# Optimization experiments

Hardware: AMD Instinct MI355X
Metric: run time of the kernel (lower is better)

## Reference

```python
import jax, jax.numpy as jnp
import numpy as np

RADIUS = 0.2
NSAMPLE = 32
BANDWIDTH = 0.1


def ellipsoid_query(xyz, new_xyz, radius, nsample):
    """xyz:(B,N,3), new_xyz:(B,P,3) -> idx:(B,P,nsample) int32.
    Ellipsoid semi-axes (radius, 2*radius, radius); first nsample hits,
    padded with the first hit (index 0 if empty), matching the CUDA kernel.
    """
    B, N, _ = xyz.shape
    inv_sq = jnp.asarray([1.0 / radius**2, 1.0 / (2.0 * radius) ** 2, 1.0 / radius**2],
                         dtype=xyz.dtype)
    # accumulate per-coordinate to avoid a (B,P,N,3) intermediate
    q = jnp.zeros((B, new_xyz.shape[1], N), dtype=xyz.dtype)
    for k in range(3):
        d = new_xyz[:, :, None, k] - xyz[:, None, :, k]  # (B,P,N)
        q = q + d * d * inv_sq[k]
    mask = q < 1.0
    cand = jnp.where(mask, jnp.arange(N, dtype=jnp.int32), jnp.int32(N))  # invalid -> N
    cand = jnp.sort(cand, axis=-1)[..., :nsample]                          # (B,P,S)
    first = cand[..., :1]
    first = jnp.where(first >= N, jnp.int32(0), first)
    return jnp.where(cand >= N, first, cand)


def group(features, idx):
    """features:(B,C,N), idx:(B,P,S) -> (B,C,P,S)"""
    return jnp.take_along_axis(features[:, :, None, :], idx[:, None, :, :], axis=-1)


def setup_inputs() -> dict:
    key = jax.random.key(0)
    k1, k2, k3 = jax.random.split(key, 3)
    xyz = jax.random.uniform(k1, (4, 8192, 3), dtype=jnp.float32)
    new_xyz = jax.random.uniform(k2, (4, 2048, 3), dtype=jnp.float32)
    features = jax.random.normal(k3, (4, 64, 8192), dtype=jnp.float32)
    return {"xyz": xyz, "new_xyz": new_xyz, "features": features}


def reference(xyz, new_xyz, features):
    idx = ellipsoid_query(xyz, new_xyz, RADIUS, NSAMPLE)          # (B,P,S)
    xyz_trans = jnp.transpose(xyz, (0, 2, 1))                      # (B,3,N)
    grouped_xyz = group(xyz_trans, idx)                            # (B,3,P,S)
    # density: gaussian of distance to center
    g = jnp.transpose(grouped_xyz, (0, 2, 3, 1))                   # (B,P,S,3)
    dist = jnp.linalg.norm(g - new_xyz[:, :, None, :], axis=-1)    # (B,P,S)
    density = jnp.exp(-dist**2 / (2.0 * BANDWIDTH**2)) / (2.5 * BANDWIDTH)
    grouped_density = (1.0 / density)[:, None, :, :]               # (B,1,P,S)
    grouped_features = group(features, idx)                        # (B,C,P,S)
    return jnp.concatenate([grouped_xyz, grouped_density, grouped_features], axis=1)
```

## Files before the change

kernel.cpp:

```cpp
#include <hip/hip_runtime.h>

constexpr int NPTS = 8192;
constexpr int NQ   = 2048;
constexpr int NC   = 64;
constexpr int NS   = 32;
constexpr int QPB  = 8;
constexpr int NCH  = 3 + 1 + NC;
constexpr int CS   = NQ * NS;


__global__ __launch_bounds__(512, 2) void ellip_query_group_kernel(
    const float* __restrict__ xyz,
    const float* __restrict__ nxyz,
    const float* __restrict__ feat,
    float* __restrict__ out)
{
    __shared__ int idx_s[QPB][NS];

    const int b    = blockIdx.y;
    const int p0   = blockIdx.x * QPB;
    const int tid  = threadIdx.x;
    const int lane = tid & 63;
    const int wave = tid >> 6;

    const float* xb = xyz + (size_t)b * NPTS * 3;

    {
        const int p = p0 + wave;
        const float qx = nxyz[((size_t)b * NQ + p) * 3 + 0];
        const float qy = nxyz[((size_t)b * NQ + p) * 3 + 1];
        const float qz = nxyz[((size_t)b * NQ + p) * 3 + 2];

        int cnt = 0;
        int first = -1;

        for (int base = 0; base < NPTS; base += 64) {
            const int i = base + lane;
            const float x = xb[i * 3 + 0];
            const float y = xb[i * 3 + 1];
            const float z = xb[i * 3 + 2];
            const float dx = __fsub_rn(qx, x);
            const float dy = __fsub_rn(qy, y);
            const float dz = __fsub_rn(qz, z);
            const float t0 = __fmul_rn(__fmul_rn(dx, dx), 25.0f);
            const float t1 = __fmul_rn(__fmul_rn(dy, dy), 6.25f);
            const float t2 = __fmul_rn(__fmul_rn(dz, dz), 25.0f);
            const float qv = __fadd_rn(__fadd_rn(t0, t1), t2);
            const bool hit = qv < 1.0f;

            const unsigned long long m = __ballot(hit);
            if (first < 0 && m != 0ull)
                first = base + __builtin_ctzll(m);
            if (hit) {
                const int pos = cnt + __popcll(m & ((1ull << lane) - 1ull));
                if (pos < NS) idx_s[wave][pos] = i;
            }
            cnt += __popcll(m);
            if (cnt >= NS) break;
        }
        if (cnt < NS) {
            const int f = (cnt == 0) ? 0 : first;
            if (lane < NS && lane >= cnt) idx_s[wave][lane] = f;
        }
    }
    __syncthreads();

    const int s = tid & 31;
    const int h = (tid >> 5) & 1;
    const int q = tid >> 6;
    const int p = p0 + q;
    const int j = idx_s[q][s];

    const float qx = nxyz[((size_t)b * NQ + p) * 3 + 0];
    const float qy = nxyz[((size_t)b * NQ + p) * 3 + 1];
    const float qz = nxyz[((size_t)b * NQ + p) * 3 + 2];
    const float px = xb[j * 3 + 0];
    const float py = xb[j * 3 + 1];
    const float pz = xb[j * 3 + 2];

    const float dx = __fsub_rn(px, qx);
    const float dy = __fsub_rn(py, qy);
    const float dz = __fsub_rn(pz, qz);
    const float d2 = __fadd_rn(__fadd_rn(__fmul_rn(dx, dx), __fmul_rn(dy, dy)),
                               __fmul_rn(dz, dz));
    const float dist = __fsqrt_rn(d2);
    const float arg  = __fdiv_rn(-__fmul_rn(dist, dist), 0.02f);
    const float density = __fmul_rn(expf(arg), 4.0f);
    const float gd = __fdiv_rn(1.0f, density);

    float* ob = out + ((size_t)b * NCH * NQ + p) * NS + s;

    if (h == 0) {
        ob[0 * (size_t)CS] = px;
        ob[2 * (size_t)CS] = pz;
    } else {
        ob[1 * (size_t)CS] = py;
        ob[3 * (size_t)CS] = gd;
    }

    const float* fb = feat + (size_t)b * NC * NPTS + j;
    #pragma unroll 4
    for (int c = h; c < NC; c += 2) {
        ob[(size_t)(4 + c) * CS] = fb[(size_t)c * NPTS];
    }
}

extern "C" void kernel_launch(void* const* d_in, const int* in_sizes, int n_in,
                              void* d_out, int out_size, void* d_ws, size_t ws_size,
                              hipStream_t stream) {
    const float* xyz  = (const float*)d_in[0];
    const float* nxyz = (const float*)d_in[1];
    const float* feat = (const float*)d_in[2];
    float* out = (float*)d_out;

    const int B = in_sizes[0] / (NPTS * 3);

    dim3 grid(NQ / QPB, B);
    dim3 block(512);
    ellip_query_group_kernel<<<grid, block, 0, stream>>>(xyz, nxyz, feat, out);
}
```

Baseline: 124.0 us.

## Pretranspose features to point-major layout for vectorized gather

Adds a transpose kernel that converts features from (B,C,N) to (B,N,C) in workspace, so the main kernel gathers each selected point's 64 channels with float4 loads from contiguous memory instead of strided scalar loads. The main kernel also changes launch bounds to 512 threads with 8 blocks per CU to raise occupancy, and keeps a direct-path fallback for when workspace is too small. The transpose adds an extra full read and write of the feature tensor plus a second launch, and the float4 path spreads each thread's stores over four channel planes.

```diff
diff --git a/kernel.cpp b/kernel.cpp
--- a/kernel.cpp
+++ b/kernel.cpp
@@ -8,69 +8,84 @@
 constexpr int NCH  = 3 + 1 + NC;
 constexpr int CS   = NQ * NS;
 
-
-__global__ __launch_bounds__(512, 2) void ellip_query_group_kernel(
-    const float* __restrict__ xyz,
-    const float* __restrict__ nxyz,
+__global__ __launch_bounds__(256, 8) void transpose_feat_kernel(
     const float* __restrict__ feat,
-    float* __restrict__ out)
-{
-    __shared__ int idx_s[QPB][NS];
-
-    const int b    = blockIdx.y;
-    const int p0   = blockIdx.x * QPB;
-    const int tid  = threadIdx.x;
-    const int lane = tid & 63;
-    const int wave = tid >> 6;
-
-    const float* xb = xyz + (size_t)b * NPTS * 3;
-
+    float* __restrict__ ftr)
+{
+    __shared__ float tile[NC][65];
+
+    const int b  = blockIdx.y;
+    const int n0 = blockIdx.x * 64;
+    const int t  = threadIdx.x;
+
+    const float* fb = feat + (size_t)b * NC * NPTS;
     {
-        const int p = p0 + wave;
-        const float qx = nxyz[((size_t)b * NQ + p) * 3 + 0];
-        const float qy = nxyz[((size_t)b * NQ + p) * 3 + 1];
-        const float qz = nxyz[((size_t)b * NQ + p) * 3 + 2];
-
-        int cnt = 0;
-        int first = -1;
-
-        for (int base = 0; base < NPTS; base += 64) {
-            const int i = base + lane;
-            const float x = xb[i * 3 + 0];
-            const float y = xb[i * 3 + 1];
-            const float z = xb[i * 3 + 2];
-            const float dx = __fsub_rn(qx, x);
-            const float dy = __fsub_rn(qy, y);
-            const float dz = __fsub_rn(qz, z);
-            const float t0 = __fmul_rn(__fmul_rn(dx, dx), 25.0f);
-            const float t1 = __fmul_rn(__fmul_rn(dy, dy), 6.25f);
-            const float t2 = __fmul_rn(__fmul_rn(dz, dz), 25.0f);
-            const float qv = __fadd_rn(__fadd_rn(t0, t1), t2);
-            const bool hit = qv < 1.0f;
-
-            const unsigned long long m = __ballot(hit);
-            if (first < 0 && m != 0ull)
-                first = base + __builtin_ctzll(m);
-            if (hit) {
-                const int pos = cnt + __popcll(m & ((1ull << lane) - 1ull));
-                if (pos < NS) idx_s[wave][pos] = i;
-            }
-            cnt += __popcll(m);
-            if (cnt >= NS) break;
+        const int pl = t & 63;
+        const int c0 = t >> 6;
+        #pragma unroll
+        for (int i = 0; i < 16; ++i) {
+            const int c = c0 + 4 * i;
+            tile[c][pl] = fb[(size_t)c * NPTS + n0 + pl];
         }
-        if (cnt < NS) {
-            const int f = (cnt == 0) ? 0 : first;
-            if (lane < NS && lane >= cnt) idx_s[wave][lane] = f;
+    }
+    __syncthreads();
+    float* tb = ftr + ((size_t)b * NPTS + n0) * NC;
+    {
+        const int cl = t & 63;
+        const int pb = t >> 6;
+        #pragma unroll
+        for (int i = 0; i < 16; ++i) {
+            const int pp = pb + 4 * i;
+            tb[(size_t)pp * NC + cl] = tile[cl][pp];
         }
     }
-    __syncthreads();
-
-    const int s = tid & 31;
-    const int h = (tid >> 5) & 1;
-    const int q = tid >> 6;
-    const int p = p0 + q;
-    const int j = idx_s[q][s];
-
+}
+
+__device__ __forceinline__ void ellipsoid_scan(
+    const float* __restrict__ xb, const float* __restrict__ nxyz,
+    int b, int p, int lane, int* __restrict__ idx_row)
+{
+    const float qx = nxyz[((size_t)b * NQ + p) * 3 + 0];
+    const float qy = nxyz[((size_t)b * NQ + p) * 3 + 1];
+    const float qz = nxyz[((size_t)b * NQ + p) * 3 + 2];
+
+    int cnt = 0;
+    int first = -1;
+
+    for (int base = 0; base < NPTS; base += 64) {
+        const int i = base + lane;
+        const float x = xb[i * 3 + 0];
+        const float y = xb[i * 3 + 1];
+        const float z = xb[i * 3 + 2];
+        const float dx = __fsub_rn(qx, x);
+        const float dy = __fsub_rn(qy, y);
+        const float dz = __fsub_rn(qz, z);
+        const float t0 = __fmul_rn(__fmul_rn(dx, dx), 25.0f);
+        const float t1 = __fmul_rn(__fmul_rn(dy, dy), 6.25f);
+        const float t2 = __fmul_rn(__fmul_rn(dz, dz), 25.0f);
+        const float qv = __fadd_rn(__fadd_rn(t0, t1), t2);
+        const bool hit = qv < 1.0f;
+
+        const unsigned long long m = __ballot(hit);
+        if (first < 0 && m != 0ull)
+            first = base + __builtin_ctzll(m);
+        if (hit) {
+            const int pos = cnt + __popcll(m & ((1ull << lane) - 1ull));
+            if (pos < NS) idx_row[pos] = i;
+        }
+        cnt += __popcll(m);
+        if (cnt >= NS) break;
+    }
+    if (cnt < NS) {
+        const int f = (cnt == 0) ? 0 : first;
+        if (lane < NS && lane >= cnt) idx_row[lane] = f;
+    }
+}
+
+__device__ __forceinline__ void write_xyz_density(
+    const float* __restrict__ xb, const float* __restrict__ nxyz,
+    int b, int p, int j, float* __restrict__ ob)
+{
     const float qx = nxyz[((size_t)b * NQ + p) * 3 + 0];
     const float qy = nxyz[((size_t)b * NQ + p) * 3 + 1];
     const float qz = nxyz[((size_t)b * NQ + p) * 3 + 2];
@@ -88,21 +103,90 @@
     const float density = __fmul_rn(expf(arg), 4.0f);
     const float gd = __fdiv_rn(1.0f, density);
 
+    ob[0 * (size_t)CS] = px;
+    ob[1 * (size_t)CS] = py;
+    ob[2 * (size_t)CS] = pz;
+    ob[3 * (size_t)CS] = gd;
+}
+
+__global__ __launch_bounds__(512, 8) void ellip_main_t_kernel(
+    const float* __restrict__ xyz,
+    const float* __restrict__ nxyz,
+    const float* __restrict__ ftr,
+    float* __restrict__ out)
+{
+    __shared__ int idx_s[QPB][NS];
+
+    const int b    = blockIdx.y;
+    const int p0   = blockIdx.x * QPB;
+    const int tid  = threadIdx.x;
+    const int lane = tid & 63;
+    const int wave = tid >> 6;
+
+    const float* xb = xyz + (size_t)b * NPTS * 3;
+
+    ellipsoid_scan(xb, nxyz, b, p0 + wave, lane, idx_s[wave]);
+    __syncthreads();
+
+    const int q = tid >> 6;
+    const int r = tid & 63;
+    const int p = p0 + q;
+    const int s = r & 31;
+    const int j = idx_s[q][s];
+
     float* ob = out + ((size_t)b * NCH * NQ + p) * NS + s;
 
-    if (h == 0) {
-        ob[0 * (size_t)CS] = px;
-        ob[2 * (size_t)CS] = pz;
-    } else {
-        ob[1 * (size_t)CS] = py;
-        ob[3 * (size_t)CS] = gd;
-    }
+    if (r < 32)
+        write_xyz_density(xb, nxyz, b, p, j, ob);
+
+    const float4* fp = (const float4*)(ftr + ((size_t)b * NPTS + j) * NC);
+    const int cg0 = r >> 5;
+    #pragma unroll
+    for (int k = 0; k < 8; ++k) {
+        const int cg = cg0 + 2 * k;
+        const float4 v = fp[cg];
+        float* oc = ob + (size_t)(4 + 4 * cg) * CS;
+        oc[0 * (size_t)CS] = v.x;
+        oc[1 * (size_t)CS] = v.y;
+        oc[2 * (size_t)CS] = v.z;
+        oc[3 * (size_t)CS] = v.w;
+    }
+}
+
+__global__ __launch_bounds__(512, 8) void ellip_main_direct_kernel(
+    const float* __restrict__ xyz,
+    const float* __restrict__ nxyz,
+    const float* __restrict__ feat,
+    float* __restrict__ out)
+{
+    __shared__ int idx_s[QPB][NS];
+
+    const int b    = blockIdx.y;
+    const int p0   = blockIdx.x * QPB;
+    const int tid  = threadIdx.x;
+    const int lane = tid & 63;
+    const int wave = tid >> 6;
+
+    const float* xb = xyz + (size_t)b * NPTS * 3;
+
+    ellipsoid_scan(xb, nxyz, b, p0 + wave, lane, idx_s[wave]);
+    __syncthreads();
+
+    const int s = tid & 31;
+    const int h = (tid >> 5) & 1;
+    const int q = tid >> 6;
+    const int p = p0 + q;
+    const int j = idx_s[q][s];
+
+    float* ob = out + ((size_t)b * NCH * NQ + p) * NS + s;
+
+    if (h == 0)
+        write_xyz_density(xb, nxyz, b, p, j, ob);
 
     const float* fb = feat + (size_t)b * NC * NPTS + j;
     #pragma unroll 4
-    for (int c = h; c < NC; c += 2) {
+    for (int c = h; c < NC; c += 2)
         ob[(size_t)(4 + c) * CS] = fb[(size_t)c * NPTS];
-    }
 }
 
 extern "C" void kernel_launch(void* const* d_in, const int* in_sizes, int n_in,
@@ -114,8 +198,13 @@
     float* out = (float*)d_out;
 
     const int B = in_sizes[0] / (NPTS * 3);
-
-    dim3 grid(NQ / QPB, B);
-    dim3 block(512);
-    ellip_query_group_kernel<<<grid, block, 0, stream>>>(xyz, nxyz, feat, out);
-}
+    const size_t trans_bytes = (size_t)B * NPTS * NC * sizeof(float);
+
+    if (ws_size >= trans_bytes) {
+        float* ftr = (float*)d_ws;
+        transpose_feat_kernel<<<dim3(NPTS / 64, B), 256, 0, stream>>>(feat, ftr);
+        ellip_main_t_kernel<<<dim3(NQ / QPB, B), 512, 0, stream>>>(xyz, nxyz, ftr, out);
+    } else {
+        ellip_main_direct_kernel<<<dim3(NQ / QPB, B), 512, 0, stream>>>(xyz, nxyz, feat, out);
+    }
+}
```

Result: faster. 113.3 us (-8.6%).
